# Performance work log

Measured on AMD Instinct MI355X. Metric: run time of the kernel, lower is better.

The kernel has to match this reference:

```python
import jax, jax.numpy as jnp
import numpy as np

D_MODEL = 1024
D_FF = 4096
N = 16384


def setup_inputs() -> dict:
    key = jax.random.key(0)
    k_b, k_w1, k_b1, k_w2, k_b2 = jax.random.split(key, 5)
    s1 = 1.0 / np.sqrt(D_MODEL)
    s2 = 1.0 / np.sqrt(D_FF)
    return {
        "batch": jax.random.normal(k_b, (N, D_MODEL), dtype=jnp.float32),
        # nn.Linear stores weight as [out_features, in_features]
        "W1": jax.random.uniform(k_w1, (D_FF, D_MODEL), jnp.float32, -s1, s1),
        "b1": jax.random.uniform(k_b1, (D_FF,), jnp.float32, -s1, s1),
        "W2": jax.random.uniform(k_w2, (D_MODEL, D_FF), jnp.float32, -s2, s2),
        "b2": jax.random.uniform(k_b2, (D_MODEL,), jnp.float32, -s2, s2),
    }


def reference(batch, W1, b1, W2, b2):
    # inner = tanh(linear1(batch)) : [N, d_ff]
    inner = jnp.tanh(batch @ W1.T + b1)
    # wx = tanh(linear2(inner)) : [N, d_model]
    wx = jnp.tanh(inner @ W2.T + b2)
    # diag(wx @ batch.T) == row-wise dot product, avoids O(N^2) matmul
    return jax.nn.sigmoid(jnp.sum(wx * batch, axis=-1))  # [N]
```

## Files before the change

### kernel.cpp

```cpp
#include <hip/hip_runtime.h>
#include <math.h>

#define N_ROWS 16384
#define DMODEL 1024
#define DFF    4096

typedef _Float16 f16;
typedef __attribute__((ext_vector_type(4))) _Float16 f16x4;
typedef __attribute__((ext_vector_type(8))) _Float16 f16x8;
typedef __attribute__((ext_vector_type(4))) float f32x4;

__device__ inline void async_ld16(const f16* g, f16* l) {
  __builtin_amdgcn_global_load_lds(
      (__attribute__((address_space(1))) void*)(g),
      (__attribute__((address_space(3))) void*)(l),
      16, 0, 0);
}

__device__ inline float fast_tanh(float x) {
  float t = __expf(2.0f * x);
  return 1.0f - 2.0f / (t + 1.0f);
}

__global__ void cast_to_f16(const float* __restrict__ src, f16* __restrict__ dst, int n) {
  int i = (blockIdx.x * blockDim.x + threadIdx.x) * 8;
  if (i >= n) return;
  float4 v0 = ((const float4*)(src + i))[0];
  float4 v1 = ((const float4*)(src + i))[1];
  f16x8 h = { (f16)v0.x, (f16)v0.y, (f16)v0.z, (f16)v0.w,
              (f16)v1.x, (f16)v1.y, (f16)v1.z, (f16)v1.w };
  *(f16x8*)(dst + i) = h;
}

#define BARRIER() __builtin_amdgcn_s_barrier()
#define WAIT_VMCNT(n) asm volatile("s_waitcnt vmcnt(" #n ")")

template <int K>
__global__ __launch_bounds__(512, 2)
void gemm256_tanh(const f16* __restrict__ A, const f16* __restrict__ B,
                  const float* __restrict__ bias, f16* __restrict__ C, int Nc) {
  extern __shared__ __align__(16) char smem[];
  f16* lds = (f16*)smem;

  const int tid  = threadIdx.x;
  const int lane = tid & 63;
  const int wave = tid >> 6;
  const int wm = (wave >> 2) * 128;
  const int wn = (wave & 3) * 64;
  const int fr = lane & 15;
  const int g  = lane >> 4;

  const int nbx = gridDim.x;
  const int nwg = nbx * gridDim.y;
  const int lin = blockIdx.y * nbx + blockIdx.x;
  const int swz = (lin & 7) * (nwg >> 3) + (lin >> 3);
  const size_t row0 = (size_t)(swz % nbx) * 256;
  const size_t col0 = (size_t)(swz / nbx) * 256;

  const int schunk = (tid & 3) ^ ((tid >> 3) & 3);
  const f16* Asrc[2]; const f16* Bsrc[2];
  const int sdst0 = tid * 8;
  const int sdst1 = 4096 + tid * 8;
  Asrc[0] = A + (row0 + (tid >> 2)) * (size_t)K + schunk * 8;
  Asrc[1] = A + (row0 + 128 + (tid >> 2)) * (size_t)K + schunk * 8;
  Bsrc[0] = B + (col0 + (tid >> 2)) * (size_t)K + schunk * 8;
  Bsrc[1] = B + (col0 + 128 + (tid >> 2)) * (size_t)K + schunk * 8;

  auto aoff = [&](int d, int kk, int m) -> int {
    const int row = wm + m * 16 + fr;
    return d * 32768 + kk * 8192 + row * 32 + (g ^ ((row >> 1) & 3)) * 8;
  };
  auto boff = [&](int d, int kk, int n) -> int {
    const int row = wn + n * 16 + fr;
    return d * 32768 + 16384 + kk * 8192 + row * 32 + (g ^ ((row >> 1) & 3)) * 8;
  };
  auto stage_unit = [&](int j, int db, int kb) {
    const int o = j & 1, kk = j >> 1;
    const int dbase = db * 32768 + o * 16384 + kk * 8192;
    async_ld16((o ? Bsrc[0] : Asrc[0]) + kb + kk * 32, lds + dbase + sdst0);
    async_ld16((o ? Bsrc[1] : Asrc[1]) + kb + kk * 32, lds + dbase + sdst1);
  };

  f32x4 acc[8][4] = {};
  constexpr int NT = K / 64;

  stage_unit(0, 0, 0);
  stage_unit(1, 0, 0);
  stage_unit(2, 0, 0);
  stage_unit(3, 0, 0);
  WAIT_VMCNT(4);
  BARRIER();

  for (int t = 0; t < NT; ++t) {
    const int d = t & 1;
    const bool pre = (t + 1) < NT;
    const int kpre = (t + 1) * 64;

    {
      f16x8 bfr[4], afr[8];
#pragma unroll
      for (int n = 0; n < 4; ++n) bfr[n] = *(const f16x8*)(lds + boff(d, 0, n));
#pragma unroll
      for (int i = 0; i < 8; ++i) afr[i] = *(const f16x8*)(lds + aoff(d, 0, i));
      if (pre) { stage_unit(0, d ^ 1, kpre); stage_unit(1, d ^ 1, kpre); }
      BARRIER();
      __builtin_amdgcn_s_setprio(1);
#pragma unroll
      for (int i = 0; i < 8; ++i)
#pragma unroll
        for (int n = 0; n < 4; ++n)
          acc[i][n] = __builtin_amdgcn_mfma_f32_16x16x32_f16(afr[i], bfr[n], acc[i][n], 0, 0, 0);
      __builtin_amdgcn_s_setprio(0);
      if (pre) { WAIT_VMCNT(4); }
      else     { WAIT_VMCNT(0); }
      BARRIER();
    }
    {
      f16x8 bfr[4], afr[8];
#pragma unroll
      for (int n = 0; n < 4; ++n) bfr[n] = *(const f16x8*)(lds + boff(d, 1, n));
#pragma unroll
      for (int i = 0; i < 8; ++i) afr[i] = *(const f16x8*)(lds + aoff(d, 1, i));
      if (pre) { stage_unit(2, d ^ 1, kpre); stage_unit(3, d ^ 1, kpre); }
      BARRIER();
      __builtin_amdgcn_s_setprio(1);
#pragma unroll
      for (int i = 0; i < 8; ++i)
#pragma unroll
        for (int n = 0; n < 4; ++n)
          acc[i][n] = __builtin_amdgcn_mfma_f32_16x16x32_f16(afr[i], bfr[n], acc[i][n], 0, 0, 0);
      __builtin_amdgcn_s_setprio(0);
      if (pre) { WAIT_VMCNT(4); }
      BARRIER();
    }
  }

#pragma unroll
  for (int m = 0; m < 8; ++m) {
#pragma unroll
    for (int n = 0; n < 4; ++n) {
      const size_t gcol = col0 + wn + n * 16 + fr;
      const float bia = bias[gcol];
      f16* Cp = C + (row0 + wm + m * 16 + g * 4) * (size_t)Nc + gcol;
#pragma unroll
      for (int r = 0; r < 4; ++r)
        Cp[(size_t)r * Nc] = (f16)fast_tanh(acc[m][n][r] + bia);
    }
  }
}

__global__ void rowdot_sigmoid(const f16* __restrict__ wx, const float* __restrict__ batch,
                               float* __restrict__ out) {
  const int row = blockIdx.x;
  const int t = threadIdx.x;
  const f16* wr = wx + (size_t)row * DMODEL + t * 4;
  const float* br = batch + (size_t)row * DMODEL + t * 4;
  f16x4 h = *(const f16x4*)wr;
  float4 b4 = *(const float4*)br;
  float s = (float)h[0] * b4.x + (float)h[1] * b4.y + (float)h[2] * b4.z + (float)h[3] * b4.w;
#pragma unroll
  for (int off = 32; off > 0; off >>= 1) s += __shfl_down(s, off, 64);
  __shared__ float partial[4];
  if ((t & 63) == 0) partial[t >> 6] = s;
  __syncthreads();
  if (t == 0) {
    float tot = partial[0] + partial[1] + partial[2] + partial[3];
    out[row] = 1.0f / (1.0f + __expf(-tot));
  }
}

extern "C" void kernel_launch(void* const* d_in, const int* in_sizes, int n_in,
                              void* d_out, int out_size, void* d_ws, size_t ws_size,
                              hipStream_t stream) {
  const float* batch = (const float*)d_in[0];
  const float* W1    = (const float*)d_in[1];
  const float* b1    = (const float*)d_in[2];
  const float* W2    = (const float*)d_in[3];
  const float* b2    = (const float*)d_in[4];
  float* out = (float*)d_out;

  char* ws = (char*)d_ws;
  f16* batch_h = (f16*)ws;  ws += (size_t)N_ROWS * DMODEL * sizeof(f16);
  f16* W1_h    = (f16*)ws;  ws += (size_t)DFF * DMODEL * sizeof(f16);
  f16* W2_h    = (f16*)ws;  ws += (size_t)DMODEL * DFF * sizeof(f16);
  f16* inner_h = (f16*)ws;  ws += (size_t)N_ROWS * DFF * sizeof(f16);
  f16* wx_h    = (f16*)ws;  ws += (size_t)N_ROWS * DMODEL * sizeof(f16);

  static bool attr_set = false;
  if (!attr_set) {
    (void)hipFuncSetAttribute((const void*)gemm256_tanh<DMODEL>,
                              hipFuncAttributeMaxDynamicSharedMemorySize, 131072);
    (void)hipFuncSetAttribute((const void*)gemm256_tanh<DFF>,
                              hipFuncAttributeMaxDynamicSharedMemorySize, 131072);
    attr_set = true;
  }

  const int nb = N_ROWS * DMODEL;
  const int nw = DFF * DMODEL;
  cast_to_f16<<<nb / 2048, 256, 0, stream>>>(batch, batch_h, nb);
  cast_to_f16<<<nw / 2048, 256, 0, stream>>>(W1, W1_h, nw);
  cast_to_f16<<<nw / 2048, 256, 0, stream>>>(W2, W2_h, nw);

  dim3 g1(N_ROWS / 256, DFF / 256);
  gemm256_tanh<DMODEL><<<g1, 512, 131072, stream>>>(batch_h, W1_h, b1, inner_h, DFF);
  dim3 g2(N_ROWS / 256, DMODEL / 256);
  gemm256_tanh<DFF><<<g2, 512, 131072, stream>>>(inner_h, W2_h, b2, wx_h, DMODEL);

  rowdot_sigmoid<<<N_ROWS, 256, 0, stream>>>(wx_h, batch, out);
}
```

Measured before the change: 434.8 us.

## Interleave LDS fragment reads with MFMA and use one barrier per k-tile

Restructures the GEMM main loop so each 64-wide k-tile issues all four prefetch units at once and has a single barrier, instead of two half-steps each with its own barrier. LDS fragment reads now go through inline-asm ds_read_b128 with manual lgkmcnt waits and sched_barrier fences. This lets reads of the second k-half overlap MFMAs on the first half. The aim is to cut barrier stalls and hide LDS latency behind matrix work. In exchange more fragment registers are live at once, and correctness now depends on hand-placed waitcnts.

```diff
diff --git a/kernel.cpp b/kernel.cpp
--- a/kernel.cpp
+++ b/kernel.cpp
@@ -15,6 +15,13 @@
       (__attribute__((address_space(1))) void*)(g),
       (__attribute__((address_space(3))) void*)(l),
       16, 0, 0);
+}
+
+__device__ inline f16x8 ds_read_b128_f16(const f16* p) {
+  f32x4 r;
+  unsigned a = (unsigned)(uintptr_t)(const __attribute__((address_space(3))) void*)p;
+  asm volatile("ds_read_b128 %0, %1" : "=v"(r) : "v"(a));
+  return __builtin_bit_cast(f16x8, r);
 }
 
 __device__ inline float fast_tanh(float x) {
@@ -34,6 +41,8 @@
 
 #define BARRIER() __builtin_amdgcn_s_barrier()
 #define WAIT_VMCNT(n) asm volatile("s_waitcnt vmcnt(" #n ")")
+#define WAIT_LGKM(n)  asm volatile("s_waitcnt lgkmcnt(" #n ")")
+#define SCHED_FENCE() __builtin_amdgcn_sched_barrier(0)
 
 template <int K>
 __global__ __launch_bounds__(512, 2)
@@ -88,7 +97,7 @@
   stage_unit(1, 0, 0);
   stage_unit(2, 0, 0);
   stage_unit(3, 0, 0);
-  WAIT_VMCNT(4);
+  WAIT_VMCNT(0);
   BARRIER();
 
   for (int t = 0; t < NT; ++t) {
@@ -96,43 +105,65 @@
     const bool pre = (t + 1) < NT;
     const int kpre = (t + 1) * 64;
 
-    {
-      f16x8 bfr[4], afr[8];
-#pragma unroll
-      for (int n = 0; n < 4; ++n) bfr[n] = *(const f16x8*)(lds + boff(d, 0, n));
-#pragma unroll
-      for (int i = 0; i < 8; ++i) afr[i] = *(const f16x8*)(lds + aoff(d, 0, i));
-      if (pre) { stage_unit(0, d ^ 1, kpre); stage_unit(1, d ^ 1, kpre); }
-      BARRIER();
-      __builtin_amdgcn_s_setprio(1);
-#pragma unroll
-      for (int i = 0; i < 8; ++i)
-#pragma unroll
-        for (int n = 0; n < 4; ++n)
-          acc[i][n] = __builtin_amdgcn_mfma_f32_16x16x32_f16(afr[i], bfr[n], acc[i][n], 0, 0, 0);
-      __builtin_amdgcn_s_setprio(0);
-      if (pre) { WAIT_VMCNT(4); }
-      else     { WAIT_VMCNT(0); }
-      BARRIER();
+    f16x8 a0[8], b0[4], a1[8], b1[4];
+
+#pragma unroll
+    for (int n = 0; n < 4; ++n) b0[n] = ds_read_b128_f16(lds + boff(d, 0, n));
+#pragma unroll
+    for (int i = 0; i < 8; ++i) a0[i] = ds_read_b128_f16(lds + aoff(d, 0, i));
+    if (pre) {
+      stage_unit(0, d ^ 1, kpre); stage_unit(1, d ^ 1, kpre);
+      stage_unit(2, d ^ 1, kpre); stage_unit(3, d ^ 1, kpre);
     }
-    {
-      f16x8 bfr[4], afr[8];
-#pragma unroll
-      for (int n = 0; n < 4; ++n) bfr[n] = *(const f16x8*)(lds + boff(d, 1, n));
-#pragma unroll
-      for (int i = 0; i < 8; ++i) afr[i] = *(const f16x8*)(lds + aoff(d, 1, i));
-      if (pre) { stage_unit(2, d ^ 1, kpre); stage_unit(3, d ^ 1, kpre); }
-      BARRIER();
-      __builtin_amdgcn_s_setprio(1);
-#pragma unroll
-      for (int i = 0; i < 8; ++i)
-#pragma unroll
-        for (int n = 0; n < 4; ++n)
-          acc[i][n] = __builtin_amdgcn_mfma_f32_16x16x32_f16(afr[i], bfr[n], acc[i][n], 0, 0, 0);
-      __builtin_amdgcn_s_setprio(0);
-      if (pre) { WAIT_VMCNT(4); }
-      BARRIER();
-    }
+#pragma unroll
+    for (int n = 0; n < 4; ++n) b1[n] = ds_read_b128_f16(lds + boff(d, 1, n));
+
+    WAIT_LGKM(4);
+    SCHED_FENCE();
+    __builtin_amdgcn_s_setprio(1);
+#pragma unroll
+    for (int i = 0; i < 4; ++i)
+#pragma unroll
+      for (int n = 0; n < 4; ++n)
+        acc[i][n] = __builtin_amdgcn_mfma_f32_16x16x32_f16(a0[i], b0[n], acc[i][n], 0, 0, 0);
+    __builtin_amdgcn_s_setprio(0);
+
+#pragma unroll
+    for (int i = 0; i < 4; ++i) a1[i] = ds_read_b128_f16(lds + aoff(d, 1, i));
+    SCHED_FENCE();
+    __builtin_amdgcn_s_setprio(1);
+#pragma unroll
+    for (int i = 4; i < 8; ++i)
+#pragma unroll
+      for (int n = 0; n < 4; ++n)
+        acc[i][n] = __builtin_amdgcn_mfma_f32_16x16x32_f16(a0[i], b0[n], acc[i][n], 0, 0, 0);
+    __builtin_amdgcn_s_setprio(0);
+
+#pragma unroll
+    for (int i = 4; i < 8; ++i) a1[i] = ds_read_b128_f16(lds + aoff(d, 1, i));
+
+    WAIT_LGKM(4);
+    SCHED_FENCE();
+    __builtin_amdgcn_s_setprio(1);
+#pragma unroll
+    for (int i = 0; i < 4; ++i)
+#pragma unroll
+      for (int n = 0; n < 4; ++n)
+        acc[i][n] = __builtin_amdgcn_mfma_f32_16x16x32_f16(a1[i], b1[n], acc[i][n], 0, 0, 0);
+    __builtin_amdgcn_s_setprio(0);
+
+    WAIT_LGKM(0);
+    SCHED_FENCE();
+    __builtin_amdgcn_s_setprio(1);
+#pragma unroll
+    for (int i = 4; i < 8; ++i)
+#pragma unroll
+      for (int n = 0; n < 4; ++n)
+        acc[i][n] = __builtin_amdgcn_mfma_f32_16x16x32_f16(a1[i], b1[n], acc[i][n], 0, 0, 0);
+    __builtin_amdgcn_s_setprio(0);
+
+    if (pre) WAIT_VMCNT(0);
+    BARRIER();
   }
 
 #pragma unroll
```

New measurement: 438.0 us. Within noise of the previous version (+0.7%).

## Restructure GEMM main loop into four-quadrant ping-pong with deeper async prefetch

Applied to the files above, without the earlier changes.

Rewrites the GEMM inner loop so each wave splits its 128x64 output into four quadrants. It loads A/B fragments from LDS in halves and interleaves MFMA clusters with barriers and lgkmcnt waits. LDS layout changes to 64-element rows with a new XOR swizzle, and staging is reorganized so the buffer for tile t+2 is prefetched into the just-consumed buffer. The aim is to overlap LDS reads, global-to-LDS loads and MFMA work more tightly, at the cost of more barriers and more intricate vmcnt accounting.

```diff
diff --git a/kernel.cpp b/kernel.cpp
--- a/kernel.cpp
+++ b/kernel.cpp
@@ -34,6 +34,7 @@
 
 #define BARRIER() __builtin_amdgcn_s_barrier()
 #define WAIT_VMCNT(n) asm volatile("s_waitcnt vmcnt(" #n ")")
+#define WAIT_LGKM(n)  asm volatile("s_waitcnt lgkmcnt(" #n ")")
 
 template <int K>
 __global__ __launch_bounds__(512, 2)
@@ -57,82 +58,123 @@
   const size_t row0 = (size_t)(swz % nbx) * 256;
   const size_t col0 = (size_t)(swz / nbx) * 256;
 
-  const int schunk = (tid & 3) ^ ((tid >> 3) & 3);
-  const f16* Asrc[2]; const f16* Bsrc[2];
-  const int sdst0 = tid * 8;
-  const int sdst1 = 4096 + tid * 8;
-  Asrc[0] = A + (row0 + (tid >> 2)) * (size_t)K + schunk * 8;
-  Asrc[1] = A + (row0 + 128 + (tid >> 2)) * (size_t)K + schunk * 8;
-  Bsrc[0] = B + (col0 + (tid >> 2)) * (size_t)K + schunk * 8;
-  Bsrc[1] = B + (col0 + 128 + (tid >> 2)) * (size_t)K + schunk * 8;
-
-  auto aoff = [&](int d, int kk, int m) -> int {
-    const int row = wm + m * 16 + fr;
-    return d * 32768 + kk * 8192 + row * 32 + (g ^ ((row >> 1) & 3)) * 8;
+  const int srow  = tid >> 3;
+  const int sslot = (tid & 7) ^ (((tid >> 5) & 1) << 1);
+  auto stage_half = [&](int op, int h, int db, int kb) {
+    const f16* src = (op ? B : A);
+    const size_t base = (op ? col0 : row0);
+#pragma unroll
+    for (int q = 0; q < 2; ++q) {
+      const f16* gp = src + (base + h * 128 + q * 64 + srow) * (size_t)K + kb + sslot * 8;
+      f16* lp = lds + db * 32768 + op * 16384 + h * 8192 + q * 4096 + tid * 8;
+      async_ld16(gp, lp);
+    }
   };
-  auto boff = [&](int d, int kk, int n) -> int {
-    const int row = wn + n * 16 + fr;
-    return d * 32768 + 16384 + kk * 8192 + row * 32 + (g ^ ((row >> 1) & 3)) * 8;
+
+  const int xr  = ((fr >> 2) & 1) << 1;
+  const int hA  = wm >> 7;
+  const int hB  = wn >> 7;
+  const int wnl = wn & 127;
+  auto aoff = [&](int d, int m, int kk) -> int {
+    return d * 32768 + hA * 8192 + (m * 16 + fr) * 64 + (((kk * 4 + g) ^ xr) * 8);
   };
-  auto stage_unit = [&](int j, int db, int kb) {
-    const int o = j & 1, kk = j >> 1;
-    const int dbase = db * 32768 + o * 16384 + kk * 8192;
-    async_ld16((o ? Bsrc[0] : Asrc[0]) + kb + kk * 32, lds + dbase + sdst0);
-    async_ld16((o ? Bsrc[1] : Asrc[1]) + kb + kk * 32, lds + dbase + sdst1);
+  auto boff = [&](int d, int n, int kk) -> int {
+    return d * 32768 + 16384 + hB * 8192 + (wnl + n * 16 + fr) * 64 + (((kk * 4 + g) ^ xr) * 8);
   };
 
   f32x4 acc[8][4] = {};
   constexpr int NT = K / 64;
 
-  stage_unit(0, 0, 0);
-  stage_unit(1, 0, 0);
-  stage_unit(2, 0, 0);
-  stage_unit(3, 0, 0);
-  WAIT_VMCNT(4);
+  stage_half(1, 0, 0, 0);  stage_half(1, 1, 0, 0);
+  stage_half(0, 0, 0, 0);  stage_half(0, 1, 0, 0);
+  stage_half(1, 0, 1, 64); stage_half(1, 1, 1, 64);
+  stage_half(0, 0, 1, 64);
+  WAIT_VMCNT(6);
   BARRIER();
 
   for (int t = 0; t < NT; ++t) {
     const int d = t & 1;
-    const bool pre = (t + 1) < NT;
-    const int kpre = (t + 1) * 64;
-
-    {
-      f16x8 bfr[4], afr[8];
-#pragma unroll
-      for (int n = 0; n < 4; ++n) bfr[n] = *(const f16x8*)(lds + boff(d, 0, n));
-#pragma unroll
-      for (int i = 0; i < 8; ++i) afr[i] = *(const f16x8*)(lds + aoff(d, 0, i));
-      if (pre) { stage_unit(0, d ^ 1, kpre); stage_unit(1, d ^ 1, kpre); }
-      BARRIER();
-      __builtin_amdgcn_s_setprio(1);
-#pragma unroll
-      for (int i = 0; i < 8; ++i)
-#pragma unroll
-        for (int n = 0; n < 4; ++n)
-          acc[i][n] = __builtin_amdgcn_mfma_f32_16x16x32_f16(afr[i], bfr[n], acc[i][n], 0, 0, 0);
-      __builtin_amdgcn_s_setprio(0);
-      if (pre) { WAIT_VMCNT(4); }
-      else     { WAIT_VMCNT(0); }
-      BARRIER();
+    const bool pre1 = (t + 1) < NT;
+    const bool pre2 = (t + 2) < NT;
+
+    f16x8 alo[4][2], ahi[4][2], blo[2][2], bhi[2][2];
+
+#pragma unroll
+    for (int n = 0; n < 2; ++n)
+#pragma unroll
+      for (int kk = 0; kk < 2; ++kk) blo[n][kk] = *(const f16x8*)(lds + boff(d, n, kk));
+#pragma unroll
+    for (int m = 0; m < 4; ++m)
+#pragma unroll
+      for (int kk = 0; kk < 2; ++kk) alo[m][kk] = *(const f16x8*)(lds + aoff(d, m, kk));
+    if (pre1) stage_half(0, 1, d ^ 1, (t + 1) * 64);
+    WAIT_LGKM(8);
+    BARRIER();
+    WAIT_LGKM(0);
+    __builtin_amdgcn_s_setprio(1);
+#pragma unroll
+    for (int kk = 0; kk < 2; ++kk)
+#pragma unroll
+      for (int m = 0; m < 4; ++m)
+#pragma unroll
+        for (int n = 0; n < 2; ++n)
+          acc[m][n] = __builtin_amdgcn_mfma_f32_16x16x32_f16(alo[m][kk], blo[n][kk], acc[m][n], 0, 0, 0);
+    __builtin_amdgcn_s_setprio(0);
+    BARRIER();
+
+#pragma unroll
+    for (int m = 0; m < 4; ++m)
+#pragma unroll
+      for (int kk = 0; kk < 2; ++kk) ahi[m][kk] = *(const f16x8*)(lds + aoff(d, 4 + m, kk));
+    BARRIER();
+    WAIT_LGKM(0);
+    __builtin_amdgcn_s_setprio(1);
+#pragma unroll
+    for (int kk = 0; kk < 2; ++kk)
+#pragma unroll
+      for (int m = 0; m < 4; ++m)
+#pragma unroll
+        for (int n = 0; n < 2; ++n)
+          acc[4 + m][n] = __builtin_amdgcn_mfma_f32_16x16x32_f16(ahi[m][kk], blo[n][kk], acc[4 + m][n], 0, 0, 0);
+    __builtin_amdgcn_s_setprio(0);
+    BARRIER();
+
+#pragma unroll
+    for (int n = 0; n < 2; ++n)
+#pragma unroll
+      for (int kk = 0; kk < 2; ++kk) bhi[n][kk] = *(const f16x8*)(lds + boff(d, 2 + n, kk));
+    BARRIER();
+    WAIT_LGKM(0);
+    __builtin_amdgcn_s_setprio(1);
+#pragma unroll
+    for (int kk = 0; kk < 2; ++kk)
+#pragma unroll
+      for (int m = 0; m < 4; ++m)
+#pragma unroll
+        for (int n = 0; n < 2; ++n)
+          acc[m][2 + n] = __builtin_amdgcn_mfma_f32_16x16x32_f16(alo[m][kk], bhi[n][kk], acc[m][2 + n], 0, 0, 0);
+    __builtin_amdgcn_s_setprio(0);
+    BARRIER();
+
+    if (pre2) {
+      const int kb2 = (t + 2) * 64;
+      stage_half(1, 0, d, kb2);
+      stage_half(1, 1, d, kb2);
+      stage_half(0, 0, d, kb2);
     }
-    {
-      f16x8 bfr[4], afr[8];
-#pragma unroll
-      for (int n = 0; n < 4; ++n) bfr[n] = *(const f16x8*)(lds + boff(d, 1, n));
-#pragma unroll
-      for (int i = 0; i < 8; ++i) afr[i] = *(const f16x8*)(lds + aoff(d, 1, i));
-      if (pre) { stage_unit(2, d ^ 1, kpre); stage_unit(3, d ^ 1, kpre); }
-      BARRIER();
-      __builtin_amdgcn_s_setprio(1);
-#pragma unroll
-      for (int i = 0; i < 8; ++i)
-#pragma unroll
-        for (int n = 0; n < 4; ++n)
-          acc[i][n] = __builtin_amdgcn_mfma_f32_16x16x32_f16(afr[i], bfr[n], acc[i][n], 0, 0, 0);
-      __builtin_amdgcn_s_setprio(0);
-      if (pre) { WAIT_VMCNT(4); }
-      BARRIER();
-    }
+    BARRIER();
+    __builtin_amdgcn_s_setprio(1);
+#pragma unroll
+    for (int kk = 0; kk < 2; ++kk)
+#pragma unroll
+      for (int m = 0; m < 4; ++m)
+#pragma unroll
+        for (int n = 0; n < 2; ++n)
+          acc[4 + m][2 + n] = __builtin_amdgcn_mfma_f32_16x16x32_f16(ahi[m][kk], bhi[n][kk], acc[4 + m][2 + n], 0, 0, 0);
+    __builtin_amdgcn_s_setprio(0);
+    if (pre2)      { WAIT_VMCNT(6); }
+    else           { WAIT_VMCNT(0); }
+    BARRIER();
   }
 
 #pragma unroll
```

After: 450.7 us. +3.7%, slower.

## Fuse row-dot into second GEMM epilogue and merge cast kernels

Applied to the files above, without the earlier changes.

The second GEMM epilogue now computes tanh(acc+bias) times the fp32 batch values, reduces across lanes, and atomically adds per-row partial sums into a zeroed accumulator. This removes the wx intermediate write/read and the separate rowdot kernel, leaving a tiny sigmoid pass. The three cast launches are merged into one kernel that also zeroes the accumulator. In exchange it adds atomics (four column tiles per row) and strided fp32 batch reads in the epilogue.

```diff
diff --git a/kernel.cpp b/kernel.cpp
--- a/kernel.cpp
+++ b/kernel.cpp
@@ -22,23 +22,39 @@
   return 1.0f - 2.0f / (t + 1.0f);
 }
 
-__global__ void cast_to_f16(const float* __restrict__ src, f16* __restrict__ dst, int n) {
-  int i = (blockIdx.x * blockDim.x + threadIdx.x) * 8;
-  if (i >= n) return;
-  float4 v0 = ((const float4*)(src + i))[0];
-  float4 v1 = ((const float4*)(src + i))[1];
+__global__ void cast_and_zero(const float* __restrict__ batch, f16* __restrict__ batch_h,
+                              const float* __restrict__ W1, f16* __restrict__ W1_h,
+                              const float* __restrict__ W2, f16* __restrict__ W2_h,
+                              float* __restrict__ rowacc) {
+  const size_t nb = (size_t)N_ROWS * DMODEL;
+  const size_t nw = (size_t)DFF * DMODEL;
+  size_t off = ((size_t)blockIdx.x * blockDim.x + threadIdx.x) * 8;
+  const float* src; f16* dst; size_t o;
+  if (off < nb) { src = batch; dst = batch_h; o = off; }
+  else if (off < nb + nw) { src = W1; dst = W1_h; o = off - nb; }
+  else if (off < nb + 2 * nw) { src = W2; dst = W2_h; o = off - nb - nw; }
+  else {
+    size_t z = off - nb - 2 * nw;
+    float4 zz = {0.f, 0.f, 0.f, 0.f};
+    ((float4*)(rowacc + z))[0] = zz;
+    ((float4*)(rowacc + z))[1] = zz;
+    return;
+  }
+  float4 v0 = ((const float4*)(src + o))[0];
+  float4 v1 = ((const float4*)(src + o))[1];
   f16x8 h = { (f16)v0.x, (f16)v0.y, (f16)v0.z, (f16)v0.w,
               (f16)v1.x, (f16)v1.y, (f16)v1.z, (f16)v1.w };
-  *(f16x8*)(dst + i) = h;
+  *(f16x8*)(dst + o) = h;
 }
 
 #define BARRIER() __builtin_amdgcn_s_barrier()
 #define WAIT_VMCNT(n) asm volatile("s_waitcnt vmcnt(" #n ")")
 
-template <int K>
+template <int K, bool FUSE>
 __global__ __launch_bounds__(512, 2)
 void gemm256_tanh(const f16* __restrict__ A, const f16* __restrict__ B,
-                  const float* __restrict__ bias, f16* __restrict__ C, int Nc) {
+                  const float* __restrict__ bias, f16* __restrict__ C, int Nc,
+                  float* __restrict__ rowacc, const float* __restrict__ batchf) {
   extern __shared__ __align__(16) char smem[];
   f16* lds = (f16*)smem;
 
@@ -135,38 +151,56 @@
     }
   }
 
-#pragma unroll
-  for (int m = 0; m < 8; ++m) {
-#pragma unroll
-    for (int n = 0; n < 4; ++n) {
-      const size_t gcol = col0 + wn + n * 16 + fr;
-      const float bia = bias[gcol];
-      f16* Cp = C + (row0 + wm + m * 16 + g * 4) * (size_t)Nc + gcol;
-#pragma unroll
-      for (int r = 0; r < 4; ++r)
-        Cp[(size_t)r * Nc] = (f16)fast_tanh(acc[m][n][r] + bia);
-    }
-  }
-}
-
-__global__ void rowdot_sigmoid(const f16* __restrict__ wx, const float* __restrict__ batch,
-                               float* __restrict__ out) {
-  const int row = blockIdx.x;
-  const int t = threadIdx.x;
-  const f16* wr = wx + (size_t)row * DMODEL + t * 4;
-  const float* br = batch + (size_t)row * DMODEL + t * 4;
-  f16x4 h = *(const f16x4*)wr;
-  float4 b4 = *(const float4*)br;
-  float s = (float)h[0] * b4.x + (float)h[1] * b4.y + (float)h[2] * b4.z + (float)h[3] * b4.w;
-#pragma unroll
-  for (int off = 32; off > 0; off >>= 1) s += __shfl_down(s, off, 64);
-  __shared__ float partial[4];
-  if ((t & 63) == 0) partial[t >> 6] = s;
-  __syncthreads();
-  if (t == 0) {
-    float tot = partial[0] + partial[1] + partial[2] + partial[3];
-    out[row] = 1.0f / (1.0f + __expf(-tot));
-  }
+  if constexpr (!FUSE) {
+#pragma unroll
+    for (int m = 0; m < 8; ++m) {
+#pragma unroll
+      for (int n = 0; n < 4; ++n) {
+        const size_t gcol = col0 + wn + n * 16 + fr;
+        const float bia = bias[gcol];
+        f16* Cp = C + (row0 + wm + m * 16 + g * 4) * (size_t)Nc + gcol;
+#pragma unroll
+        for (int r = 0; r < 4; ++r)
+          Cp[(size_t)r * Nc] = (f16)fast_tanh(acc[m][n][r] + bia);
+      }
+    }
+  } else {
+    float rsum[8][4];
+#pragma unroll
+    for (int m = 0; m < 8; ++m)
+#pragma unroll
+      for (int r = 0; r < 4; ++r) rsum[m][r] = 0.f;
+#pragma unroll
+    for (int m = 0; m < 8; ++m) {
+#pragma unroll
+      for (int n = 0; n < 4; ++n) {
+        const size_t gcol = col0 + wn + n * 16 + fr;
+        const float bia = bias[gcol];
+        const float* bp = batchf + (row0 + wm + m * 16 + g * 4) * DMODEL + gcol;
+#pragma unroll
+        for (int r = 0; r < 4; ++r)
+          rsum[m][r] += fast_tanh(acc[m][n][r] + bia) * bp[(size_t)r * DMODEL];
+      }
+    }
+#pragma unroll
+    for (int m = 0; m < 8; ++m) {
+#pragma unroll
+      for (int r = 0; r < 4; ++r) {
+        float s = rsum[m][r];
+        s += __shfl_xor(s, 1, 64);
+        s += __shfl_xor(s, 2, 64);
+        s += __shfl_xor(s, 4, 64);
+        s += __shfl_xor(s, 8, 64);
+        if (fr == 0)
+          atomicAdd(&rowacc[row0 + wm + m * 16 + g * 4 + r], s);
+      }
+    }
+  }
+}
+
+__global__ void sigmoid_rows(const float* __restrict__ rowacc, float* __restrict__ out) {
+  const int i = blockIdx.x * blockDim.x + threadIdx.x;
+  out[i] = 1.0f / (1.0f + __expf(-rowacc[i]));
 }
 
 extern "C" void kernel_launch(void* const* d_in, const int* in_sizes, int n_in,
@@ -180,31 +214,33 @@
   float* out = (float*)d_out;
 
   char* ws = (char*)d_ws;
-  f16* batch_h = (f16*)ws;  ws += (size_t)N_ROWS * DMODEL * sizeof(f16);
-  f16* W1_h    = (f16*)ws;  ws += (size_t)DFF * DMODEL * sizeof(f16);
-  f16* W2_h    = (f16*)ws;  ws += (size_t)DMODEL * DFF * sizeof(f16);
-  f16* inner_h = (f16*)ws;  ws += (size_t)N_ROWS * DFF * sizeof(f16);
-  f16* wx_h    = (f16*)ws;  ws += (size_t)N_ROWS * DMODEL * sizeof(f16);
+  f16* batch_h  = (f16*)ws;   ws += (size_t)N_ROWS * DMODEL * sizeof(f16);
+  f16* W1_h     = (f16*)ws;   ws += (size_t)DFF * DMODEL * sizeof(f16);
+  f16* W2_h     = (f16*)ws;   ws += (size_t)DMODEL * DFF * sizeof(f16);
+  f16* inner_h  = (f16*)ws;   ws += (size_t)N_ROWS * DFF * sizeof(f16);
+  float* rowacc = (float*)ws; ws += (size_t)N_ROWS * sizeof(float);
 
   static bool attr_set = false;
   if (!attr_set) {
-    (void)hipFuncSetAttribute((const void*)gemm256_tanh<DMODEL>,
+    (void)hipFuncSetAttribute((const void*)gemm256_tanh<DMODEL, false>,
                               hipFuncAttributeMaxDynamicSharedMemorySize, 131072);
-    (void)hipFuncSetAttribute((const void*)gemm256_tanh<DFF>,
+    (void)hipFuncSetAttribute((const void*)gemm256_tanh<DFF, true>,
                               hipFuncAttributeMaxDynamicSharedMemorySize, 131072);
     attr_set = true;
   }
 
-  const int nb = N_ROWS * DMODEL;
-  const int nw = DFF * DMODEL;
-  cast_to_f16<<<nb / 2048, 256, 0, stream>>>(batch, batch_h, nb);
-  cast_to_f16<<<nw / 2048, 256, 0, stream>>>(W1, W1_h, nw);
-  cast_to_f16<<<nw / 2048, 256, 0, stream>>>(W2, W2_h, nw);
+  const size_t nb = (size_t)N_ROWS * DMODEL;
+  const size_t nw = (size_t)DFF * DMODEL;
+  const int total_thr = (int)((nb + 2 * nw) / 8 + N_ROWS / 8);
+  cast_and_zero<<<total_thr / 256, 256, 0, stream>>>(batch, batch_h, W1, W1_h,
+                                                     W2, W2_h, rowacc);
 
   dim3 g1(N_ROWS / 256, DFF / 256);
-  gemm256_tanh<DMODEL><<<g1, 512, 131072, stream>>>(batch_h, W1_h, b1, inner_h, DFF);
+  gemm256_tanh<DMODEL, false><<<g1, 512, 131072, stream>>>(
+      batch_h, W1_h, b1, inner_h, DFF, nullptr, nullptr);
   dim3 g2(N_ROWS / 256, DMODEL / 256);
-  gemm256_tanh<DFF><<<g2, 512, 131072, stream>>>(inner_h, W2_h, b2, wx_h, DMODEL);
-
-  rowdot_sigmoid<<<N_ROWS, 256, 0, stream>>>(wx_h, batch, out);
-}
+  gemm256_tanh<DFF, true><<<g2, 512, 131072, stream>>>(
+      inner_h, W2_h, b2, nullptr, DMODEL, rowacc, batch);
+
+  sigmoid_rows<<<N_ROWS / 256, 256, 0, stream>>>(rowacc, out);
+}
```

Measured after the change: 434.9 us. About the same (+0.0%).
